# Kernel tuning notes

Measured on AMD Instinct MI355X. Metric: run time of the kernel, lower is better.

The kernel has to match this reference:

```python
import jax, jax.numpy as jnp
import numpy as np

D_MODEL = 1024
D_HID = 1408
N_SHARED = 2
N_ROUTED = 8
TOP_K = 2
B, S = 2, 1024
EPS = float(jnp.finfo(jnp.float32).eps)  # torch RMSNorm eps=None -> finfo eps


def setup_inputs() -> dict:
    key = jax.random.key(0)
    ks = jax.random.split(key, 8)
    b1 = 1.0 / np.sqrt(D_MODEL)  # uniform bound for W1 (1/sqrt(d_input))
    b2 = 1.0 / np.sqrt(D_MODEL)  # uniform bound for W2 (1/sqrt(d_output))
    return {
        "x": jax.random.normal(ks[0], (B, S, D_MODEL), dtype=jnp.float32),
        "norm_w": jnp.ones((D_MODEL,), dtype=jnp.float32),
        "Wr": jax.random.uniform(ks[1], (N_ROUTED, D_MODEL), minval=-b1, maxval=b1, dtype=jnp.float32),
        "Ws1": jax.random.uniform(ks[2], (N_SHARED, D_MODEL, D_HID), minval=-b1, maxval=b1, dtype=jnp.float32),
        "bs1": jnp.zeros((N_SHARED, 1, D_HID), dtype=jnp.float32),
        "Ws2": jax.random.uniform(ks[3], (N_SHARED, D_HID, D_MODEL), minval=-b2, maxval=b2, dtype=jnp.float32),
        "bs2": jnp.zeros((N_SHARED, 1, D_MODEL), dtype=jnp.float32),
        "W1": jax.random.uniform(ks[4], (N_ROUTED, D_MODEL, D_HID), minval=-b1, maxval=b1, dtype=jnp.float32),
        "b1": jnp.zeros((N_ROUTED, 1, D_HID), dtype=jnp.float32),
        "W2": jax.random.uniform(ks[5], (N_ROUTED, D_HID, D_MODEL), minval=-b2, maxval=b2, dtype=jnp.float32),
        "b2": jnp.zeros((N_ROUTED, 1, D_MODEL), dtype=jnp.float32),
    }


def _rmsnorm(x, w):
    ms = jnp.mean(jnp.square(x), axis=-1, keepdims=True)
    return x * jax.lax.rsqrt(ms + EPS) * w


def reference(x, norm_w, Wr, Ws1, bs1, Ws2, bs2, W1, b1, W2, b2):
    inputs = _rmsnorm(x, norm_w)  # (B,S,d)

    # Shared experts: sum over all shared experts of SwiGLU-FFN
    hs = jax.nn.silu(jnp.einsum("bsd,edh->besh", inputs, Ws1) + bs1[:, None])  # (B,E_s,S,h)
    shared_out = jnp.einsum("besh,ehd->bsd", hs, Ws2) + jnp.sum(bs2[:, None], axis=0)  # (B,S,d)

    # Router (no bias, ver V2: affinity = raw logits)
    raw_aff = jnp.einsum("bsd,ed->bse", inputs, Wr)  # (B,S,E)
    _, idx = jax.lax.top_k(raw_aff, TOP_K)  # (B,S,K)

    # Routed experts: dropout=0, so computing all experts then gathering outputs
    # equals the source's per-token weight-gather math.
    hr = jax.nn.silu(jnp.einsum("bsd,edh->bseh", inputs, W1) + b1[:, 0])  # (B,S,E,h)
    out_all = jnp.einsum("bseh,ehd->bsed", hr, W2) + b2[:, 0]  # (B,S,E,d)

    out_k = jnp.take_along_axis(out_all, idx[..., None], axis=2)  # (B,S,K,d)
    aff_k = jnp.take_along_axis(raw_aff, idx, axis=-1)  # (B,S,K)
    routed_out = jnp.einsum("bsk,bskd->bsd", aff_k, out_k)

    return x + shared_out + routed_out
```

## Files before the change

### kernel.cpp

```cpp
#include <hip/hip_runtime.h>
#include <hip/hip_bf16.h>
#include <stdint.h>


#define NTOK 2048
#define DM   1024
#define DH   1408
#define DHP  1536
#define NGRP 10
#define EPSV 1.1920928955078125e-7f
#define MAXTILES 40
#define MAXSLOTS (MAXTILES * 256)
#define MT128 (MAXSLOTS / 128)

typedef __bf16 bf16x8 __attribute__((ext_vector_type(8)));
typedef float  f32x4  __attribute__((ext_vector_type(4)));
typedef unsigned short u16x8 __attribute__((ext_vector_type(8)));

__device__ __forceinline__ void async16(const void* g, void* l) {
  __builtin_amdgcn_global_load_lds(
      (const __attribute__((address_space(1))) unsigned*)g,
      (__attribute__((address_space(3))) unsigned*)l, 16, 0, 0);
}

__device__ __forceinline__ unsigned lds_off(const void* p) {
  return (unsigned)(unsigned long long)(const __attribute__((address_space(3))) char*)p;
}

__device__ __forceinline__ unsigned short f2bf(float f) {
  unsigned u = __builtin_bit_cast(unsigned, f);
  unsigned r = (u + 0x7FFFu + ((u >> 16) & 1u)) >> 16;
  return (unsigned short)r;
}
__device__ __forceinline__ float bf2f(unsigned short h) {
  unsigned u = ((unsigned)h) << 16;
  return __builtin_bit_cast(float, u);
}

__device__ __forceinline__ float4 ntload4(const float* p) {
  const f32x4* vp = (const f32x4*)p;
  f32x4 v = __builtin_nontemporal_load(vp);
  float4 r;
  r.x = v[0]; r.y = v[1]; r.z = v[2]; r.w = v[3];
  return r;
}

__device__ __forceinline__ int xcd_swizzle(int id, int nwg) {
  int q = nwg >> 3;
  return (id & 7) * q + (id >> 3);
}

#define TRN_BLKS 3520
__global__ __launch_bounds__(256) void prep_k(
    const float* __restrict__ Ws1, const float* __restrict__ W1,
    const float* __restrict__ Ws2, const float* __restrict__ W2,
    unsigned short* __restrict__ W1t, unsigned short* __restrict__ W2t,
    const float* __restrict__ x, const float* __restrict__ nw,
    const float* __restrict__ Wr, unsigned short* __restrict__ xb,
    int* __restrict__ idx2, float* __restrict__ gate2) {
  __shared__ unsigned short Lt[64 * 132];
  __shared__ float ps[4];
  __shared__ float pw[32];
  int bi = blockIdx.x;
  int tid = threadIdx.x;
  if (bi < TRN_BLKS) {
    const float* s; unsigned short* d; int C, Kd, k0, n0;
    if (bi < 1760) {
      int z = bi / 176, rem = bi % 176, kb = rem / 11, nb = rem % 11;
      C = DH; Kd = DM; k0 = kb * 64; n0 = nb * 128;
      s = (z < 2) ? Ws1 + (size_t)z * DM * DH : W1 + (size_t)(z - 2) * DM * DH;
      d = W1t + (size_t)z * DHP * DM;
    } else {
      int b2 = bi - 1760;
      int z = b2 / 176, rem = b2 % 176, kb = rem / 8, nb = rem % 8;
      C = DM; Kd = DH; k0 = kb * 64; n0 = nb * 128;
      s = (z < 2) ? Ws2 + (size_t)z * DH * DM : W2 + (size_t)(z - 2) * DH * DM;
      d = W2t + (size_t)z * DM * DH;
    }
#pragma unroll
    for (int p = 0; p < 8; ++p) {
      int kr = p * 8 + (tid >> 5);
      int nc = (tid & 31) * 4;
      float4 v = ntload4(s + (size_t)(k0 + kr) * C + n0 + nc);
      int ncs = nc ^ ((kr >> 3) << 2);
      ushort4 u;
      u.x = f2bf(v.x); u.y = f2bf(v.y); u.z = f2bf(v.z); u.w = f2bf(v.w);
      *(ushort4*)(&Lt[kr * 132 + ncs]) = u;
    }
    __syncthreads();
#pragma unroll
    for (int p = 0; p < 4; ++p) {
      int chunk = p * 256 + tid;
      int n = chunk >> 3, kc = (chunk & 7) * 8;
      int nswz = n ^ ((chunk & 7) << 2);
      u16x8 uv;
#pragma unroll
      for (int j = 0; j < 8; ++j) uv[j] = Lt[(kc + j) * 132 + nswz];
      *(u16x8*)(d + (size_t)(n0 + n) * Kd + k0 + kc) = uv;
    }
    return;
  }
  int t = bi - TRN_BLKS;
  const float4 v = *(const float4*)(x + (size_t)t * DM + tid * 4);
  float s = v.x * v.x + v.y * v.y + v.z * v.z + v.w * v.w;
#pragma unroll
  for (int o = 32; o; o >>= 1) s += __shfl_down(s, o);
  if ((tid & 63) == 0) ps[tid >> 6] = s;
  __syncthreads();
  float tot = ps[0] + ps[1] + ps[2] + ps[3];
  float r = rsqrtf(tot * (1.0f / (float)DM) + EPSV);
  const float4 wv = *(const float4*)(nw + tid * 4);
  float4 y;
  y.x = v.x * r * wv.x; y.y = v.y * r * wv.y; y.z = v.z * r * wv.z; y.w = v.w * r * wv.w;
  ushort4 u; u.x = f2bf(y.x); u.y = f2bf(y.y); u.z = f2bf(y.z); u.w = f2bf(y.w);
  *(ushort4*)(xb + (size_t)t * DM + tid * 4) = u;
  float pr[8];
#pragma unroll
  for (int e = 0; e < 8; ++e) {
    const float4 w4 = *(const float4*)(Wr + (size_t)e * DM + tid * 4);
    pr[e] = y.x * w4.x + y.y * w4.y + y.z * w4.z + y.w * w4.w;
  }
#pragma unroll
  for (int e = 0; e < 8; ++e)
#pragma unroll
    for (int o = 32; o; o >>= 1) pr[e] += __shfl_down(pr[e], o);
  if ((tid & 63) == 0) {
    int w = tid >> 6;
#pragma unroll
    for (int e = 0; e < 8; ++e) pw[w * 8 + e] = pr[e];
  }
  __syncthreads();
  if (tid == 0) {
    float af[8];
#pragma unroll
    for (int e = 0; e < 8; ++e) af[e] = pw[e] + pw[8 + e] + pw[16 + e] + pw[24 + e];
    int e1 = 0; float a1 = af[0];
#pragma unroll
    for (int e = 1; e < 8; ++e) if (af[e] > a1) { a1 = af[e]; e1 = e; }
    int e2 = -1; float a2 = -3.4e38f;
#pragma unroll
    for (int e = 0; e < 8; ++e) if (e != e1 && af[e] > a2) { a2 = af[e]; e2 = e; }
    idx2[t * 2] = e1; idx2[t * 2 + 1] = e2;
    gate2[t * 2] = a1; gate2[t * 2 + 1] = a2;
  }
}

__global__ __launch_bounds__(256) void buildplace_k(
    const int* __restrict__ idx2, const float* __restrict__ gate2,
    const float* __restrict__ bs1, const float* __restrict__ b1,
    const float* __restrict__ bs2, const float* __restrict__ b2,
    int* __restrict__ tile_group, int* __restrict__ tok_list,
    float* __restrict__ gate_list, int* __restrict__ slot_of,
    float* __restrict__ b1p, float* __restrict__ b2p) {
  __shared__ int cnt_s[8], base_s[8], fill_s[8];
  int tid = threadIdx.x;
  if (tid < 8) { cnt_s[tid] = 0; fill_s[tid] = 0; }
  __syncthreads();
  for (int t = tid; t < NTOK; t += 256) {
    atomicAdd(&cnt_s[idx2[2 * t]], 1);
    atomicAdd(&cnt_s[idx2[2 * t + 1]], 1);
  }
  __syncthreads();
  if (tid == 0) {
    int tile = 16;
    for (int e = 0; e < 8; ++e) {
      base_s[e] = tile * 256;
      tile += (cnt_s[e] + 255) >> 8;
    }
    for (int i = 0; i < 16; ++i) tile_group[i] = i >> 3;
    int tt = 16;
    for (int e = 0; e < 8; ++e) {
      int nt = (cnt_s[e] + 255) >> 8;
      for (int i = 0; i < nt; ++i) tile_group[tt++] = 2 + e;
    }
    for (; tt < MAXTILES; ++tt) tile_group[tt] = -1;
  }
  for (int s = tid; s < MAXSLOTS; s += 256) {
    int tok; float gv;
    if (s < 2048)      { tok = s;        gv = 1.f; }
    else if (s < 4096) { tok = s - 2048; gv = 1.f; }
    else               { tok = -1;       gv = 0.f; }
    tok_list[s] = tok; gate_list[s] = gv;
  }
  for (int i = tid; i < NGRP * DH; i += 256) {
    int g = i / DH, j = i % DH;
    b1p[i] = (g < 2) ? bs1[g * DH + j] : b1[(g - 2) * DH + j];
  }
  for (int i = tid; i < NGRP * DM; i += 256) {
    int g = i >> 10, j = i & (DM - 1);
    b2p[i] = (g < 2) ? bs2[g * DM + j] : b2[(g - 2) * DM + j];
  }
  __syncthreads();
  for (int t = tid; t < NTOK; t += 256) {
#pragma unroll
    for (int k = 0; k < 2; ++k) {
      int e = idx2[t * 2 + k];
      int pos = atomicAdd(&fill_s[e], 1);
      int slot = base_s[e] + pos;
      tok_list[slot] = t;
      gate_list[slot] = gate2[t * 2 + k];
      slot_of[t * 2 + k] = slot;
    }
  }
}

#define DSR(dst, addr) asm volatile("ds_read_b128 %0, %1" : "=v"(dst) : "v"(addr))

template <int KD, int ND, int NBN, bool FIRST>
__global__ __launch_bounds__(256, 2) void gemm_k(
    const unsigned short* __restrict__ A, const int* __restrict__ tok_list,
    const int* __restrict__ tile_group, const unsigned short* __restrict__ Bt,
    const float* __restrict__ biasP, const float* __restrict__ gate_list,
    unsigned short* __restrict__ Out) {
  constexpr int NK = KD / 64;
  int wg = xcd_swizzle(blockIdx.x, MT128 * NBN);
  int mt = wg / NBN, bn = (wg % NBN) * 128;
  int g = tile_group[mt >> 1];
  if (g < 0) return;
  int tid = threadIdx.x;
  __shared__ unsigned short As[2][128 * 64];
  __shared__ unsigned short Bs[2][128 * 64];
  __shared__ int rows_s[128];
  __shared__ float gates_s[128];
  if (tid < 128) {
    if (FIRST) {
      int tok = tok_list[mt * 128 + tid];
      rows_s[tid] = tok < 0 ? 0 : tok;
    } else {
      gates_s[tid] = gate_list[mt * 128 + tid];
    }
  }
  __syncthreads();
  int drow = tid >> 3, schk = tid & 7;
  const unsigned short* aS[4];
  const unsigned short* bS[4];
#pragma unroll
  for (int p = 0; p < 4; ++p) {
    int rl = p * 32 + drow;
    int arow = FIRST ? rows_s[rl] : mt * 128 + rl;
    int sc = schk ^ (rl & 7);
    aS[p] = A + (size_t)arow * KD + sc * 8;
    bS[p] = Bt + ((size_t)g * ND + bn + rl) * KD + sc * 8;
  }
  int lane = tid & 63, w = tid >> 6;
  int wm = w >> 1, wn = w & 1;
  int lr = lane & 15, hi = lane >> 4;
  int aOff[4], bOff[4];
#pragma unroll
  for (int q = 0; q < 4; ++q) {
    int row = wm * 64 + q * 16 + lr;
    aOff[q] = row * 128 + ((hi ^ (row & 7)) << 4);
  }
#pragma unroll
  for (int nf = 0; nf < 4; ++nf) {
    int row = wn * 64 + nf * 16 + lr;
    bOff[nf] = row * 128 + ((hi ^ (row & 7)) << 4);
  }
  unsigned aBase[2] = {lds_off(&As[0][0]), lds_off(&As[1][0])};
  unsigned bBase[2] = {lds_off(&Bs[0][0]), lds_off(&Bs[1][0])};
  float bv[4];
#pragma unroll
  for (int nf = 0; nf < 4; ++nf) {
    int col = bn + wn * 64 + nf * 16 + lr;
    int cidx = (!FIRST || col < DH) ? col : 0;
    bv[nf] = biasP[g * (FIRST ? DH : DM) + cidx];
    asm volatile("" : "+v"(bv[nf]));
  }
  f32x4 acc[4][4];
#pragma unroll
  for (int q = 0; q < 4; ++q)
#pragma unroll
    for (int nf = 0; nf < 4; ++nf) acc[q][nf] = (f32x4){0.f, 0.f, 0.f, 0.f};
  auto stage = [&](int buf, int kt) {
#pragma unroll
    for (int p = 0; p < 4; ++p) {
      async16(aS[p] + kt * 64, (char*)&As[buf][0] + p * 4096 + tid * 16);
      async16(bS[p] + kt * 64, (char*)&Bs[buf][0] + p * 4096 + tid * 16);
    }
  };
  asm volatile("s_waitcnt vmcnt(0)" ::: "memory");
  __builtin_amdgcn_sched_barrier(0);
  stage(0, 0);
  __builtin_amdgcn_sched_barrier(0);
  int cur = 0;
  for (int kt = 0; kt < NK; ++kt) {
    if (kt + 1 < NK) {
      __builtin_amdgcn_sched_barrier(0);
      stage(cur ^ 1, kt + 1);
      __builtin_amdgcn_sched_barrier(0);
      asm volatile("s_waitcnt vmcnt(8)" ::: "memory");
      __builtin_amdgcn_sched_barrier(0);
    } else {
      asm volatile("s_waitcnt vmcnt(0)" ::: "memory");
      __builtin_amdgcn_sched_barrier(0);
    }
    asm volatile("s_barrier" ::: "memory");
#pragma unroll
    for (int ks = 0; ks < 2; ++ks) {
      int kx = ks ? 64 : 0;
      f32x4 ar[4], br[4];
#pragma unroll
      for (int q = 0; q < 4; ++q) {
        unsigned ad = aBase[cur] + (unsigned)(aOff[q] ^ kx);
        DSR(ar[q], ad);
      }
#pragma unroll
      for (int nf = 0; nf < 4; ++nf) {
        unsigned bd = bBase[cur] + (unsigned)(bOff[nf] ^ kx);
        DSR(br[nf], bd);
      }
      asm volatile("s_waitcnt lgkmcnt(0)" ::: "memory");
      __builtin_amdgcn_sched_barrier(0);
      __builtin_amdgcn_s_setprio(1);
#pragma unroll
      for (int q = 0; q < 4; ++q)
#pragma unroll
        for (int nf = 0; nf < 4; ++nf)
          acc[q][nf] = __builtin_amdgcn_mfma_f32_16x16x32_bf16(
              __builtin_bit_cast(bf16x8, ar[q]), __builtin_bit_cast(bf16x8, br[nf]),
              acc[q][nf], 0, 0, 0);
      __builtin_amdgcn_s_setprio(0);
    }
    asm volatile("s_barrier" ::: "memory");
    cur ^= 1;
  }
#pragma unroll
  for (int nf = 0; nf < 4; ++nf) {
    int col = bn + wn * 64 + nf * 16 + lr;
    if (!FIRST || col < DH) {
#pragma unroll
      for (int q = 0; q < 4; ++q) {
        int rl = wm * 64 + q * 16 + hi * 4;
#pragma unroll
        for (int j = 0; j < 4; ++j) {
          float v = acc[q][nf][j] + bv[nf];
          if (FIRST) {
            v = v / (1.f + expf(-v));
            Out[(size_t)(mt * 128 + rl + j) * DH + col] = f2bf(v);
          } else {
            v *= gates_s[rl + j];
            Out[(size_t)(mt * 128 + rl + j) * DM + col] = f2bf(v);
          }
        }
      }
    }
  }
}

__global__ __launch_bounds__(256) void combine_k(
    const float* __restrict__ x, const unsigned short* __restrict__ O,
    const int* __restrict__ slot_of, float* __restrict__ out) {
  int t = blockIdx.x, tid = threadIdx.x;
  int d = tid * 4;
  int s0 = slot_of[t * 2], s1 = slot_of[t * 2 + 1];
  float4 xv = *(const float4*)(x + (size_t)t * DM + d);
  ushort4 a = *(const ushort4*)(O + (size_t)t * DM + d);
  ushort4 b = *(const ushort4*)(O + (size_t)(2048 + t) * DM + d);
  ushort4 c = *(const ushort4*)(O + (size_t)s0 * DM + d);
  ushort4 e = *(const ushort4*)(O + (size_t)s1 * DM + d);
  float4 o;
  o.x = xv.x + bf2f(a.x) + bf2f(b.x) + bf2f(c.x) + bf2f(e.x);
  o.y = xv.y + bf2f(a.y) + bf2f(b.y) + bf2f(c.y) + bf2f(e.y);
  o.z = xv.z + bf2f(a.z) + bf2f(b.z) + bf2f(c.z) + bf2f(e.z);
  o.w = xv.w + bf2f(a.w) + bf2f(b.w) + bf2f(c.w) + bf2f(e.w);
  *(float4*)(out + (size_t)t * DM + d) = o;
}

extern "C" void kernel_launch(void* const* d_in, const int* in_sizes, int n_in,
                              void* d_out, int out_size, void* d_ws, size_t ws_size,
                              hipStream_t stream) {
  const float* x   = (const float*)d_in[0];
  const float* nw  = (const float*)d_in[1];
  const float* Wr  = (const float*)d_in[2];
  const float* Ws1 = (const float*)d_in[3];
  const float* bs1 = (const float*)d_in[4];
  const float* Ws2 = (const float*)d_in[5];
  const float* bs2 = (const float*)d_in[6];
  const float* W1  = (const float*)d_in[7];
  const float* b1  = (const float*)d_in[8];
  const float* W2  = (const float*)d_in[9];
  const float* b2  = (const float*)d_in[10];
  float* out = (float*)d_out;

  char* ws = (char*)d_ws;
  size_t off = 0;
  auto alloc = [&](size_t n) {
    size_t r = off;
    off += (n + 255) & ~(size_t)255;
    return r;
  };
  unsigned short* XnB  = (unsigned short*)(ws + alloc((size_t)NTOK * DM * 2));
  unsigned short* W1t  = (unsigned short*)(ws + alloc((size_t)NGRP * DHP * DM * 2));
  unsigned short* W2t  = (unsigned short*)(ws + alloc((size_t)NGRP * DM * DH * 2));
  unsigned short* Hb   = (unsigned short*)(ws + alloc((size_t)MAXSLOTS * DH * 2));
  unsigned short* Ob   = (unsigned short*)(ws + alloc((size_t)MAXSLOTS * DM * 2));
  int*   idx2      = (int*)(ws + alloc((size_t)NTOK * 2 * 4));
  float* gate2     = (float*)(ws + alloc((size_t)NTOK * 2 * 4));
  int*   tile_group= (int*)(ws + alloc(64 * 4));
  int*   tok_list  = (int*)(ws + alloc((size_t)MAXSLOTS * 4));
  float* gate_list = (float*)(ws + alloc((size_t)MAXSLOTS * 4));
  int*   slot_of   = (int*)(ws + alloc((size_t)NTOK * 2 * 4));
  float* b1p       = (float*)(ws + alloc((size_t)NGRP * DH * 4));
  float* b2p       = (float*)(ws + alloc((size_t)NGRP * DM * 4));

  prep_k<<<TRN_BLKS + NTOK, 256, 0, stream>>>(Ws1, W1, Ws2, W2, W1t, W2t,
                                              x, nw, Wr, XnB, idx2, gate2);
  buildplace_k<<<1, 256, 0, stream>>>(idx2, gate2, bs1, b1, bs2, b2,
                                      tile_group, tok_list, gate_list, slot_of, b1p, b2p);
  gemm_k<DM, DHP, 12, true><<<MT128 * 12, 256, 0, stream>>>(
      XnB, tok_list, tile_group, W1t, b1p, nullptr, Hb);
  gemm_k<DH, DM, 8, false><<<MT128 * 8, 256, 0, stream>>>(
      Hb, tok_list, tile_group, W2t, b2p, gate_list, Ob);
  combine_k<<<NTOK, 256, 0, stream>>>(x, Ob, slot_of, out);
}
```

Baseline: 151.1 us.

## Overlap W2 transpose with first GEMM and batch LDS reads per k-tile

The W2/Ws2 fp32-to-bf16 transpose blocks move out of the prep kernel and are appended to the first expert GEMM launch as extra blocks. They can then run alongside the GEMM1 tiles instead of sitting on the critical path before the router. The GEMM inner loop now issues all LDS reads for both k-halves up front and waits on a partial lgkmcnt, so the second half's reads overlap the first half's MFMAs. The cost is more live registers and shared memory now carved manually from a byte array.

```diff
diff --git a/kernel.cpp b/kernel.cpp
--- a/kernel.cpp
+++ b/kernel.cpp
@@ -12,6 +12,7 @@
 #define MAXTILES 40
 #define MAXSLOTS (MAXTILES * 256)
 #define MT128 (MAXSLOTS / 128)
+#define SMEM_BYTES (66048 + 512)
 
 typedef __bf16 bf16x8 __attribute__((ext_vector_type(8)));
 typedef float  f32x4  __attribute__((ext_vector_type(4)));
@@ -50,11 +51,35 @@
   return (id & 7) * q + (id >> 3);
 }
 
-#define TRN_BLKS 3520
+__device__ __forceinline__ void transpose_role(
+    const float* s, unsigned short* d, int C, int Kd, int k0, int n0,
+    unsigned short* Lt, int tid) {
+#pragma unroll
+  for (int p = 0; p < 8; ++p) {
+    int kr = p * 8 + (tid >> 5);
+    int nc = (tid & 31) * 4;
+    float4 v = ntload4(s + (size_t)(k0 + kr) * C + n0 + nc);
+    int ncs = nc ^ ((kr >> 3) << 2);
+    ushort4 u;
+    u.x = f2bf(v.x); u.y = f2bf(v.y); u.z = f2bf(v.z); u.w = f2bf(v.w);
+    *(ushort4*)(&Lt[kr * 132 + ncs]) = u;
+  }
+  __syncthreads();
+#pragma unroll
+  for (int p = 0; p < 4; ++p) {
+    int chunk = p * 256 + tid;
+    int n = chunk >> 3, kc = (chunk & 7) * 8;
+    int nswz = n ^ ((chunk & 7) << 2);
+    u16x8 uv;
+#pragma unroll
+    for (int j = 0; j < 8; ++j) uv[j] = Lt[(kc + j) * 132 + nswz];
+    *(u16x8*)(d + (size_t)(n0 + n) * Kd + k0 + kc) = uv;
+  }
+}
+
 __global__ __launch_bounds__(256) void prep_k(
     const float* __restrict__ Ws1, const float* __restrict__ W1,
-    const float* __restrict__ Ws2, const float* __restrict__ W2,
-    unsigned short* __restrict__ W1t, unsigned short* __restrict__ W2t,
+    unsigned short* __restrict__ W1t,
     const float* __restrict__ x, const float* __restrict__ nw,
     const float* __restrict__ Wr, unsigned short* __restrict__ xb,
     int* __restrict__ idx2, float* __restrict__ gate2) {
@@ -63,44 +88,14 @@
   __shared__ float pw[32];
   int bi = blockIdx.x;
   int tid = threadIdx.x;
-  if (bi < TRN_BLKS) {
-    const float* s; unsigned short* d; int C, Kd, k0, n0;
-    if (bi < 1760) {
-      int z = bi / 176, rem = bi % 176, kb = rem / 11, nb = rem % 11;
-      C = DH; Kd = DM; k0 = kb * 64; n0 = nb * 128;
-      s = (z < 2) ? Ws1 + (size_t)z * DM * DH : W1 + (size_t)(z - 2) * DM * DH;
-      d = W1t + (size_t)z * DHP * DM;
-    } else {
-      int b2 = bi - 1760;
-      int z = b2 / 176, rem = b2 % 176, kb = rem / 8, nb = rem % 8;
-      C = DM; Kd = DH; k0 = kb * 64; n0 = nb * 128;
-      s = (z < 2) ? Ws2 + (size_t)z * DH * DM : W2 + (size_t)(z - 2) * DH * DM;
-      d = W2t + (size_t)z * DM * DH;
-    }
-#pragma unroll
-    for (int p = 0; p < 8; ++p) {
-      int kr = p * 8 + (tid >> 5);
-      int nc = (tid & 31) * 4;
-      float4 v = ntload4(s + (size_t)(k0 + kr) * C + n0 + nc);
-      int ncs = nc ^ ((kr >> 3) << 2);
-      ushort4 u;
-      u.x = f2bf(v.x); u.y = f2bf(v.y); u.z = f2bf(v.z); u.w = f2bf(v.w);
-      *(ushort4*)(&Lt[kr * 132 + ncs]) = u;
-    }
-    __syncthreads();
-#pragma unroll
-    for (int p = 0; p < 4; ++p) {
-      int chunk = p * 256 + tid;
-      int n = chunk >> 3, kc = (chunk & 7) * 8;
-      int nswz = n ^ ((chunk & 7) << 2);
-      u16x8 uv;
-#pragma unroll
-      for (int j = 0; j < 8; ++j) uv[j] = Lt[(kc + j) * 132 + nswz];
-      *(u16x8*)(d + (size_t)(n0 + n) * Kd + k0 + kc) = uv;
-    }
+  if (bi < 1760) {
+    int z = bi / 176, rem = bi % 176, kb = rem / 11, nb = rem % 11;
+    const float* s = (z < 2) ? Ws1 + (size_t)z * DM * DH : W1 + (size_t)(z - 2) * DM * DH;
+    unsigned short* d = W1t + (size_t)z * DHP * DM;
+    transpose_role(s, d, DH, DM, kb * 64, nb * 128, Lt, tid);
     return;
   }
-  int t = bi - TRN_BLKS;
+  int t = bi - 1760;
   const float4 v = *(const float4*)(x + (size_t)t * DM + tid * 4);
   float s = v.x * v.x + v.y * v.y + v.z * v.z + v.w * v.w;
 #pragma unroll
@@ -207,21 +202,21 @@
 #define DSR(dst, addr) asm volatile("ds_read_b128 %0, %1" : "=v"(dst) : "v"(addr))
 
 template <int KD, int ND, int NBN, bool FIRST>
-__global__ __launch_bounds__(256, 2) void gemm_k(
+__device__ __forceinline__ void gemm_body(
+    int wg, char* smem,
     const unsigned short* __restrict__ A, const int* __restrict__ tok_list,
     const int* __restrict__ tile_group, const unsigned short* __restrict__ Bt,
     const float* __restrict__ biasP, const float* __restrict__ gate_list,
     unsigned short* __restrict__ Out) {
   constexpr int NK = KD / 64;
-  int wg = xcd_swizzle(blockIdx.x, MT128 * NBN);
   int mt = wg / NBN, bn = (wg % NBN) * 128;
   int g = tile_group[mt >> 1];
   if (g < 0) return;
   int tid = threadIdx.x;
-  __shared__ unsigned short As[2][128 * 64];
-  __shared__ unsigned short Bs[2][128 * 64];
-  __shared__ int rows_s[128];
-  __shared__ float gates_s[128];
+  unsigned short (*As)[128 * 64] = (unsigned short (*)[128 * 64])smem;
+  unsigned short (*Bs)[128 * 64] = (unsigned short (*)[128 * 64])(smem + 32768);
+  int* rows_s = (int*)(smem + 65536);
+  float* gates_s = (float*)(smem + 66048);
   if (tid < 128) {
     if (FIRST) {
       int tok = tok_list[mt * 128 + tid];
@@ -295,32 +290,37 @@
       __builtin_amdgcn_sched_barrier(0);
     }
     asm volatile("s_barrier" ::: "memory");
-#pragma unroll
-    for (int ks = 0; ks < 2; ++ks) {
-      int kx = ks ? 64 : 0;
-      f32x4 ar[4], br[4];
-#pragma unroll
-      for (int q = 0; q < 4; ++q) {
-        unsigned ad = aBase[cur] + (unsigned)(aOff[q] ^ kx);
-        DSR(ar[q], ad);
-      }
-#pragma unroll
-      for (int nf = 0; nf < 4; ++nf) {
-        unsigned bd = bBase[cur] + (unsigned)(bOff[nf] ^ kx);
-        DSR(br[nf], bd);
-      }
-      asm volatile("s_waitcnt lgkmcnt(0)" ::: "memory");
-      __builtin_amdgcn_sched_barrier(0);
-      __builtin_amdgcn_s_setprio(1);
-#pragma unroll
-      for (int q = 0; q < 4; ++q)
-#pragma unroll
-        for (int nf = 0; nf < 4; ++nf)
-          acc[q][nf] = __builtin_amdgcn_mfma_f32_16x16x32_bf16(
-              __builtin_bit_cast(bf16x8, ar[q]), __builtin_bit_cast(bf16x8, br[nf]),
-              acc[q][nf], 0, 0, 0);
-      __builtin_amdgcn_s_setprio(0);
-    }
+    f32x4 ar0[4], br0[4], ar1[4], br1[4];
+#pragma unroll
+    for (int q = 0; q < 4; ++q) DSR(ar0[q], aBase[cur] + (unsigned)aOff[q]);
+#pragma unroll
+    for (int nf = 0; nf < 4; ++nf) DSR(br0[nf], bBase[cur] + (unsigned)bOff[nf]);
+#pragma unroll
+    for (int q = 0; q < 4; ++q) DSR(ar1[q], aBase[cur] + (unsigned)(aOff[q] ^ 64));
+#pragma unroll
+    for (int nf = 0; nf < 4; ++nf) DSR(br1[nf], bBase[cur] + (unsigned)(bOff[nf] ^ 64));
+    asm volatile("s_waitcnt lgkmcnt(8)" ::: "memory");
+    __builtin_amdgcn_sched_barrier(0);
+    __builtin_amdgcn_s_setprio(1);
+#pragma unroll
+    for (int q = 0; q < 4; ++q)
+#pragma unroll
+      for (int nf = 0; nf < 4; ++nf)
+        acc[q][nf] = __builtin_amdgcn_mfma_f32_16x16x32_bf16(
+            __builtin_bit_cast(bf16x8, ar0[q]), __builtin_bit_cast(bf16x8, br0[nf]),
+            acc[q][nf], 0, 0, 0);
+    __builtin_amdgcn_s_setprio(0);
+    asm volatile("s_waitcnt lgkmcnt(0)" ::: "memory");
+    __builtin_amdgcn_sched_barrier(0);
+    __builtin_amdgcn_s_setprio(1);
+#pragma unroll
+    for (int q = 0; q < 4; ++q)
+#pragma unroll
+      for (int nf = 0; nf < 4; ++nf)
+        acc[q][nf] = __builtin_amdgcn_mfma_f32_16x16x32_bf16(
+            __builtin_bit_cast(bf16x8, ar1[q]), __builtin_bit_cast(bf16x8, br1[nf]),
+            acc[q][nf], 0, 0, 0);
+    __builtin_amdgcn_s_setprio(0);
     asm volatile("s_barrier" ::: "memory");
     cur ^= 1;
   }
@@ -345,6 +345,36 @@
       }
     }
   }
+}
+
+__global__ __launch_bounds__(256, 2) void gemm1t_k(
+    const unsigned short* __restrict__ A, const int* __restrict__ tok_list,
+    const int* __restrict__ tile_group, const unsigned short* __restrict__ Bt,
+    const float* __restrict__ b1p, unsigned short* __restrict__ Hb,
+    const float* __restrict__ Ws2, const float* __restrict__ W2,
+    unsigned short* __restrict__ W2t) {
+  __shared__ char smem[SMEM_BYTES];
+  int bi = blockIdx.x;
+  if (bi >= MT128 * 12) {
+    int b2 = bi - MT128 * 12;
+    int z = b2 / 176, rem = b2 % 176, kb = rem / 8, nb = rem % 8;
+    const float* s = (z < 2) ? Ws2 + (size_t)z * DH * DM : W2 + (size_t)(z - 2) * DH * DM;
+    unsigned short* d = W2t + (size_t)z * DM * DH;
+    transpose_role(s, d, DM, DH, kb * 64, nb * 128, (unsigned short*)smem, threadIdx.x);
+    return;
+  }
+  int wg = xcd_swizzle(bi, MT128 * 12);
+  gemm_body<DM, DHP, 12, true>(wg, smem, A, tok_list, tile_group, Bt, b1p, nullptr, Hb);
+}
+
+__global__ __launch_bounds__(256, 2) void gemm2_k(
+    const unsigned short* __restrict__ A, const int* __restrict__ tok_list,
+    const int* __restrict__ tile_group, const unsigned short* __restrict__ Bt,
+    const float* __restrict__ b2p, const float* __restrict__ gate_list,
+    unsigned short* __restrict__ Ob) {
+  __shared__ char smem[SMEM_BYTES];
+  int wg = xcd_swizzle(blockIdx.x, MT128 * 8);
+  gemm_body<DH, DM, 8, false>(wg, smem, A, tok_list, tile_group, Bt, b2p, gate_list, Ob);
 }
 
 __global__ __launch_bounds__(256) void combine_k(
@@ -403,13 +433,12 @@
   float* b1p       = (float*)(ws + alloc((size_t)NGRP * DH * 4));
   float* b2p       = (float*)(ws + alloc((size_t)NGRP * DM * 4));
 
-  prep_k<<<TRN_BLKS + NTOK, 256, 0, stream>>>(Ws1, W1, Ws2, W2, W1t, W2t,
-                                              x, nw, Wr, XnB, idx2, gate2);
+  prep_k<<<1760 + NTOK, 256, 0, stream>>>(Ws1, W1, W1t, x, nw, Wr, XnB, idx2, gate2);
   buildplace_k<<<1, 256, 0, stream>>>(idx2, gate2, bs1, b1, bs2, b2,
                                       tile_group, tok_list, gate_list, slot_of, b1p, b2p);
-  gemm_k<DM, DHP, 12, true><<<MT128 * 12, 256, 0, stream>>>(
-      XnB, tok_list, tile_group, W1t, b1p, nullptr, Hb);
-  gemm_k<DH, DM, 8, false><<<MT128 * 8, 256, 0, stream>>>(
+  gemm1t_k<<<MT128 * 12 + 1760, 256, 0, stream>>>(
+      XnB, tok_list, tile_group, W1t, b1p, Hb, Ws2, W2, W2t);
+  gemm2_k<<<MT128 * 8, 256, 0, stream>>>(
       Hb, tok_list, tile_group, W2t, b2p, gate_list, Ob);
   combine_k<<<NTOK, 256, 0, stream>>>(x, Ob, slot_of, out);
 }
```

Result: faster. 145.3 us (-3.8%).
